# Optimization experiments

Measured on AMD Instinct MI355X. Metric: run time of the kernel, lower is better.

## Reference

```python
import jax, jax.numpy as jnp
import numpy as np

N_NODES = 100000


def _gcn_conv(x, W, b, src, dst, norm):
    # x: [N, Fin] -> [N, Fout]; PyG GCNConv: linear, normalized scatter-add, bias
    x = x @ W
    msgs = x[src] * norm[:, None]  # gather + edge scale
    out = jax.ops.segment_sum(msgs, dst, num_segments=N_NODES)
    return out + b


def setup_inputs() -> dict:
    key = jax.random.key(0)
    ks = jax.random.split(key, 8)
    N, E, F, H, C = N_NODES, 600000, 128, 128, 40
    s = lambda fan: 1.0 / np.sqrt(fan)
    return {
        "features": jax.random.normal(ks[0], (N, F), dtype=jnp.float32),
        "edge_index": jax.random.randint(ks[1], (2, E), 0, N, dtype=jnp.int64),
        "W1": jax.random.normal(ks[2], (F, H), dtype=jnp.float32) * s(F),
        "b1": jnp.zeros((H,), dtype=jnp.float32),
        "W2": jax.random.normal(ks[3], (H, H), dtype=jnp.float32) * s(H),
        "b2": jnp.zeros((H,), dtype=jnp.float32),
        "W3": jax.random.normal(ks[4], (H, C), dtype=jnp.float32) * s(H),
        "b3": jnp.zeros((C,), dtype=jnp.float32),
    }


def reference(features, edge_index, W1, b1, W2, b2, W3, b3):
    N = N_NODES
    # add self-loops (PyG GCNConv default)
    loops = jnp.arange(N, dtype=edge_index.dtype)
    src = jnp.concatenate([edge_index[0], loops])
    dst = jnp.concatenate([edge_index[1], loops])
    # symmetric normalization: deg^-1/2[src] * deg^-1/2[dst]
    deg = jax.ops.segment_sum(jnp.ones_like(dst, dtype=features.dtype), dst,
                              num_segments=N)
    dis = jnp.where(deg > 0, jax.lax.rsqrt(jnp.maximum(deg, 1.0)), 0.0)
    norm = dis[src] * dis[dst]

    x = jax.nn.relu(_gcn_conv(features, W1, b1, src, dst, norm))
    x = jax.nn.relu(_gcn_conv(x, W2, b2, src, dst, norm))
    x = jax.nn.relu(_gcn_conv(x, W3, b3, src, dst, norm))
    return jax.nn.log_softmax(x, axis=-1)
```

## Files before the change

kernel.cpp:

```cpp
#include <hip/hip_runtime.h>
#include <hip/hip_bf16.h>

#define NN 100000
#define NE 600000
#define NBLK 391
#define NPAD 100096

typedef unsigned int uint;
typedef unsigned short ushort;
typedef __attribute__((ext_vector_type(8))) short bf16x8;
typedef __attribute__((ext_vector_type(4))) float f32x4;

__device__ __forceinline__ ushort f2b(float f) {
    union { float f; uint u; } v; v.f = f;
    return (ushort)((v.u + 0x7fffu + ((v.u >> 16) & 1u)) >> 16);
}
__device__ __forceinline__ uint f2b2(float lo, float hi) {
    return (uint)f2b(lo) | ((uint)f2b(hi) << 16);
}
__device__ __forceinline__ float b2f(uint h) {
    union { uint u; float f; } v; v.u = h << 16; return v.f;
}

__global__ __launch_bounds__(256) void k_cnt_init(int* __restrict__ cnt) {
    int i = blockIdx.x * 256 + threadIdx.x;
    if (i < NN) cnt[i] = 0;
}
__global__ __launch_bounds__(256) void k_cnt(const int* __restrict__ dst,
                                             int* __restrict__ cnt,
                                             int* __restrict__ rank) {
    int e = blockIdx.x * 256 + threadIdx.x;
    if (e < NE) rank[e] = atomicAdd(&cnt[dst[e]], 1);
}
__global__ __launch_bounds__(256) void k_blockred(const int* __restrict__ cnt,
                                                  int* __restrict__ blocksum) {
    int t = threadIdx.x;
    int i = blockIdx.x * 256 + t;
    int c = (i < NN) ? cnt[i] : 0;
    #pragma unroll
    for (int o = 32; o; o >>= 1) c += __shfl_xor(c, o, 64);
    __shared__ int ws[4];
    if ((t & 63) == 0) ws[t >> 6] = c;
    __syncthreads();
    if (t == 0) blocksum[blockIdx.x] = ws[0] + ws[1] + ws[2] + ws[3];
}
__global__ __launch_bounds__(256) void k_scanblk_castW(const int* __restrict__ blocksum,
                                                       int* __restrict__ blockbase,
                                                       const float* __restrict__ W1,
                                                       const float* __restrict__ W2,
                                                       const float* __restrict__ W3,
                                                       ushort* __restrict__ WTall) {
    int t = threadIdx.x;
    if (blockIdx.x == 0) {
        __shared__ int s[NBLK];
        for (int i = t; i < NBLK; i += 256) s[i] = blocksum[i];
        __syncthreads();
        if (t == 0) {
            int run = 0;
            for (int i = 0; i < NBLK; ++i) { int v = s[i]; s[i] = run; run += v; }
        }
        __syncthreads();
        for (int i = t; i < NBLK; i += 256) blockbase[i] = s[i];
    } else {
        int o = (blockIdx.x - 1) * 256 + t;
        if (o >= 38912) return;
        float v;
        if (o < 32768) {
            const float* W = (o < 16384) ? W1 : W2;
            int off = o & 16383;
            int n = off >> 7, k = off & 127;
            v = W[k * 128 + n];
        } else {
            int off = o - 32768;
            int n = off >> 7, k = off & 127;
            v = (n < 40) ? W3[k * 40 + n] : 0.f;
        }
        WTall[o] = f2b(v);
    }
}
__global__ __launch_bounds__(256) void k_offsets(const int* __restrict__ cnt,
                                                 const int* __restrict__ blockbase,
                                                 int* __restrict__ offsets,
                                                 float* __restrict__ dis) {
    int t = threadIdx.x, lane = t & 63, wv = t >> 6;
    int i = blockIdx.x * 256 + t;
    int c = (i < NN) ? cnt[i] : 0;
    int x = c;
    #pragma unroll
    for (int o = 1; o < 64; o <<= 1) {
        int v = __shfl_up(x, o, 64);
        if (lane >= o) x += v;
    }
    __shared__ int wsum[4], wbase[4];
    if (lane == 63) wsum[wv] = x;
    __syncthreads();
    if (t == 0) {
        int run = 0;
        #pragma unroll
        for (int k = 0; k < 4; ++k) { wbase[k] = run; run += wsum[k]; }
    }
    __syncthreads();
    int excl = blockbase[blockIdx.x] + wbase[wv] + x - c;
    if (i < NN) {
        offsets[i] = excl;
        dis[i] = rsqrtf((float)(c + 1));
        if (i == NN - 1) offsets[NN] = excl + c;
    }
}
__global__ __launch_bounds__(256) void k_fill(const int* __restrict__ src,
                                              const int* __restrict__ dst,
                                              const int* __restrict__ rank,
                                              const int* __restrict__ offsets,
                                              int* __restrict__ edges) {
    int e = blockIdx.x * 256 + threadIdx.x;
    if (e < NE) {
        int s = src[e], d = dst[e], r = rank[e];
        edges[offsets[d] + r] = s;
    }
}

template <bool F32IN>
__global__ __launch_bounds__(256) void k_gemm128b(const void* __restrict__ Xin,
                                                  const ushort* __restrict__ WT,
                                                  const float* __restrict__ dis,
                                                  ushort* __restrict__ Yb) {
    __shared__ ushort AL[64 * 136];
    __shared__ ushort BL[128 * 136];
    const int t = threadIdx.x;
    const int rbase = blockIdx.x * 64;
    if (blockIdx.x == 0 && t < 16) {
        uint4 z = make_uint4(0, 0, 0, 0);
        ((uint4*)(Yb + (size_t)NN * 128))[t] = z;
    }
    #pragma unroll
    for (int i = 0; i < 8; ++i) {
        int ch = t + 256 * i;
        int n = ch >> 4, c = ch & 15;
        *(int4*)(BL + n * 136 + c * 8) = *(const int4*)(WT + n * 128 + c * 8);
    }
    #pragma unroll
    for (int i = 0; i < 4; ++i) {
        int ch = t + 256 * i;
        int m = ch >> 4, c = ch & 15;
        int row = min(rbase + m, NN - 1);
        if (F32IN) {
            const float* Xf = (const float*)Xin;
            float4 f0 = *(const float4*)(Xf + (size_t)row * 128 + c * 8);
            float4 f1 = *(const float4*)(Xf + (size_t)row * 128 + c * 8 + 4);
            uint4 o;
            o.x = f2b2(f0.x, f0.y);
            o.y = f2b2(f0.z, f0.w);
            o.z = f2b2(f1.x, f1.y);
            o.w = f2b2(f1.z, f1.w);
            *(uint4*)(AL + m * 136 + c * 8) = o;
        } else {
            const ushort* Xb = (const ushort*)Xin;
            *(int4*)(AL + m * 136 + c * 8) =
                *(const int4*)(Xb + (size_t)row * 128 + c * 8);
        }
    }
    __syncthreads();
    const int wv = t >> 6, l = t & 63;
    const int m16 = l & 15, q = l >> 4;
    f32x4 acc[8];
    #pragma unroll
    for (int j = 0; j < 8; ++j) acc[j] = (f32x4){0.f, 0.f, 0.f, 0.f};
    #pragma unroll
    for (int kt = 0; kt < 4; ++kt) {
        bf16x8 a = *(const bf16x8*)(AL + (wv * 16 + m16) * 136 + kt * 32 + q * 8);
        #pragma unroll
        for (int j = 0; j < 8; ++j) {
            bf16x8 b = *(const bf16x8*)(BL + (j * 16 + m16) * 136 + kt * 32 + q * 8);
            acc[j] = __builtin_amdgcn_mfma_f32_16x16x32_bf16(a, b, acc[j], 0, 0, 0);
        }
    }
    #pragma unroll
    for (int r = 0; r < 4; ++r) {
        int row = rbase + wv * 16 + q * 4 + r;
        if (row < NN) {
            float ds = dis[row];
            #pragma unroll
            for (int j = 0; j < 8; ++j)
                Yb[(size_t)row * 128 + j * 16 + m16] = f2b(acc[j][r] * ds);
        }
    }
}

__global__ __launch_bounds__(256) void k_gemm40b(const ushort* __restrict__ Xb,
                                                 const ushort* __restrict__ W3T,
                                                 const float* __restrict__ dis,
                                                 ushort* __restrict__ Yb) {
    __shared__ ushort AL[128 * 136];
    __shared__ ushort BL[48 * 136];
    const int t = threadIdx.x;
    const int rbase = blockIdx.x * 128;
    if (blockIdx.x == 0 && t < 8) {
        uint4 z = make_uint4(0, 0, 0, 0);
        ((uint4*)(Yb + (size_t)NN * 64))[t] = z;
    }
    #pragma unroll
    for (int i = 0; i < 3; ++i) {
        int ch = t + 256 * i;
        int n = ch >> 4, c = ch & 15;
        *(int4*)(BL + n * 136 + c * 8) = *(const int4*)(W3T + n * 128 + c * 8);
    }
    #pragma unroll
    for (int i = 0; i < 8; ++i) {
        int ch = t + 256 * i;
        int m = ch >> 4, c = ch & 15;
        int row = min(rbase + m, NN - 1);
        *(int4*)(AL + m * 136 + c * 8) =
            *(const int4*)(Xb + (size_t)row * 128 + c * 8);
    }
    __syncthreads();
    const int wv = t >> 6, l = t & 63;
    const int m16 = l & 15, q = l >> 4;
    f32x4 acc[2][3];
    #pragma unroll
    for (int i = 0; i < 2; ++i)
        #pragma unroll
        for (int j = 0; j < 3; ++j) acc[i][j] = (f32x4){0.f, 0.f, 0.f, 0.f};
    #pragma unroll
    for (int kt = 0; kt < 4; ++kt) {
        bf16x8 a[2], b[3];
        #pragma unroll
        for (int i = 0; i < 2; ++i)
            a[i] = *(const bf16x8*)(AL + ((wv * 2 + i) * 16 + m16) * 136 + kt * 32 + q * 8);
        #pragma unroll
        for (int j = 0; j < 3; ++j)
            b[j] = *(const bf16x8*)(BL + (j * 16 + m16) * 136 + kt * 32 + q * 8);
        #pragma unroll
        for (int i = 0; i < 2; ++i)
            #pragma unroll
            for (int j = 0; j < 3; ++j)
                acc[i][j] = __builtin_amdgcn_mfma_f32_16x16x32_bf16(a[i], b[j], acc[i][j], 0, 0, 0);
    }
    #pragma unroll
    for (int i = 0; i < 2; ++i) {
        #pragma unroll
        for (int r = 0; r < 4; ++r) {
            int row = rbase + (wv * 2 + i) * 16 + q * 4 + r;
            if (row < NN) {
                float ds = dis[row];
                #pragma unroll
                for (int j = 0; j < 3; ++j)
                    Yb[(size_t)row * 64 + j * 16 + m16] = f2b(acc[i][j][r] * ds);
            }
        }
    }
}

__global__ __launch_bounds__(256) void k_agg128b(const int* __restrict__ offsets,
                                                 const int* __restrict__ edges,
                                                 const float* __restrict__ dis,
                                                 const ushort* __restrict__ xw,
                                                 const float* __restrict__ bias,
                                                 ushort* __restrict__ out) {
    const int t = threadIdx.x;
    const int wv = t >> 6, lane = t & 63;
    const int hl = lane & 15;
    const int qsel = lane & 48;
    const int n = (blockIdx.x * 4 + wv) * 4 + (lane >> 4);
    const bool nvalid = n < NN;
    const int nc = nvalid ? n : NN - 1;
    const int beg = offsets[nc], end = offsets[nc + 1];
    const int deg = end - beg;
    int s_l = (hl < deg) ? edges[beg + hl] : NN;
    uint4 v0 = ((const uint4*)(xw + (size_t)nc * 128))[hl];
    float a0 = b2f(v0.x & 0xffffu), a1 = b2f(v0.x >> 16);
    float a2 = b2f(v0.y & 0xffffu), a3 = b2f(v0.y >> 16);
    float a4 = b2f(v0.z & 0xffffu), a5 = b2f(v0.z >> 16);
    float a6 = b2f(v0.w & 0xffffu), a7 = b2f(v0.w >> 16);
    int degc = min(deg, 16);
    int m1 = max(degc, __shfl_xor(degc, 16, 64));
    int dmax = max(m1, __shfl_xor(m1, 32, 64));
    int jceil = (dmax + 7) & ~7;
    for (int j = 0; j < jceil; j += 8) {
        int s[8]; uint4 u[8];
        #pragma unroll
        for (int k = 0; k < 8; ++k) s[k] = __shfl(s_l, qsel + j + k, 64);
        #pragma unroll
        for (int k = 0; k < 8; ++k)
            u[k] = ((const uint4*)(xw + (size_t)s[k] * 128))[hl];
        #pragma unroll
        for (int k = 0; k < 8; ++k) {
            a0 += b2f(u[k].x & 0xffffu); a1 += b2f(u[k].x >> 16);
            a2 += b2f(u[k].y & 0xffffu); a3 += b2f(u[k].y >> 16);
            a4 += b2f(u[k].z & 0xffffu); a5 += b2f(u[k].z >> 16);
            a6 += b2f(u[k].w & 0xffffu); a7 += b2f(u[k].w >> 16);
        }
    }
    for (int jj = beg + 16; jj < end; ++jj) {
        int s2 = edges[jj];
        uint4 u = ((const uint4*)(xw + (size_t)s2 * 128))[hl];
        a0 += b2f(u.x & 0xffffu); a1 += b2f(u.x >> 16);
        a2 += b2f(u.y & 0xffffu); a3 += b2f(u.y >> 16);
        a4 += b2f(u.z & 0xffffu); a5 += b2f(u.z >> 16);
        a6 += b2f(u.w & 0xffffu); a7 += b2f(u.w >> 16);
    }
    float d = dis[nc];
    float4 bv0 = ((const float4*)bias)[2 * hl];
    float4 bv1 = ((const float4*)bias)[2 * hl + 1];
    a0 = fmaxf(fmaf(a0, d, bv0.x), 0.f); a1 = fmaxf(fmaf(a1, d, bv0.y), 0.f);
    a2 = fmaxf(fmaf(a2, d, bv0.z), 0.f); a3 = fmaxf(fmaf(a3, d, bv0.w), 0.f);
    a4 = fmaxf(fmaf(a4, d, bv1.x), 0.f); a5 = fmaxf(fmaf(a5, d, bv1.y), 0.f);
    a6 = fmaxf(fmaf(a6, d, bv1.z), 0.f); a7 = fmaxf(fmaf(a7, d, bv1.w), 0.f);
    if (nvalid) {
        uint4 o;
        o.x = f2b2(a0, a1);
        o.y = f2b2(a2, a3);
        o.z = f2b2(a4, a5);
        o.w = f2b2(a6, a7);
        ((uint4*)(out + (size_t)n * 128))[hl] = o;
    }
}

__global__ __launch_bounds__(256) void k_agg40_lsm(const int* __restrict__ offsets,
                                                   const int* __restrict__ edges,
                                                   const float* __restrict__ dis,
                                                   const ushort* __restrict__ xw,
                                                   const float* __restrict__ bias,
                                                   float* __restrict__ out) {
    const int t = threadIdx.x;
    const int wv = t >> 6, lane = t & 63;
    const int hl = lane & 31;
    const int hsel = lane & 32;
    const int n = (blockIdx.x * 4 + wv) * 2 + (lane >> 5);
    const bool nvalid = n < NN;
    const int nc = nvalid ? n : NN - 1;
    const bool act = hl < 20;
    const int beg = offsets[nc], end = offsets[nc + 1];
    const int deg = end - beg;
    int s_l = (hl < deg) ? edges[beg + hl] : NN;
    uint v0 = ((const uint*)(xw + (size_t)nc * 64))[hl];
    float x0 = b2f(v0 & 0xffffu);
    float x1 = b2f(v0 >> 16);
    int degc = min(deg, 32);
    int dmax = max(degc, __shfl_xor(degc, 32, 64));
    int jceil = (dmax + 7) & ~7;
    for (int j = 0; j < jceil; j += 8) {
        int s[8]; uint u[8];
        #pragma unroll
        for (int k = 0; k < 8; ++k) s[k] = __shfl(s_l, hsel + j + k, 64);
        #pragma unroll
        for (int k = 0; k < 8; ++k)
            u[k] = ((const uint*)(xw + (size_t)s[k] * 64))[hl];
        #pragma unroll
        for (int k = 0; k < 8; ++k) {
            x0 += b2f(u[k] & 0xffffu);
            x1 += b2f(u[k] >> 16);
        }
    }
    for (int jj = beg + 32; jj < end; ++jj) {
        int s2 = edges[jj];
        uint u = ((const uint*)(xw + (size_t)s2 * 64))[hl];
        x0 += b2f(u & 0xffffu);
        x1 += b2f(u >> 16);
    }
    float d = dis[nc];
    if (act) {
        float2 bv = ((const float2*)bias)[hl];
        x0 = fmaxf(fmaf(x0, d, bv.x), 0.f);
        x1 = fmaxf(fmaf(x1, d, bv.y), 0.f);
    }
    float m = act ? fmaxf(x0, x1) : -1e30f;
    #pragma unroll
    for (int o = 16; o; o >>= 1) m = fmaxf(m, __shfl_xor(m, o, 64));
    float e = act ? (expf(x0 - m) + expf(x1 - m)) : 0.f;
    #pragma unroll
    for (int o = 16; o; o >>= 1) e += __shfl_xor(e, o, 64);
    if (act && nvalid) {
        float lg = m + logf(e);
        float2 o2 = make_float2(x0 - lg, x1 - lg);
        *(float2*)(out + (size_t)n * 40 + 2 * hl) = o2;
    }
}

extern "C" void kernel_launch(void* const* d_in, const int* in_sizes, int n_in,
                              void* d_out, int out_size, void* d_ws, size_t ws_size,
                              hipStream_t stream) {
    const float* feat = (const float*)d_in[0];
    const int* ei = (const int*)d_in[1];
    const float* W1 = (const float*)d_in[2];
    const float* b1 = (const float*)d_in[3];
    const float* W2 = (const float*)d_in[4];
    const float* b2 = (const float*)d_in[5];
    const float* W3 = (const float*)d_in[6];
    const float* b3 = (const float*)d_in[7];
    const int* src = ei;
    const int* dst = ei + NE;
    float* out = (float*)d_out;

    char* w = (char*)d_ws;
    int* cnt = (int*)w;        w += 100352 * 4;
    float* dis = (float*)w;    w += 100352 * 4;
    int* offsets = (int*)w;    w += 100608 * 4;
    int* rank = (int*)w;       w += 600064 * 4;
    int* blocksum = (int*)w;   w += 512 * 4;
    int* blockbase = (int*)w;  w += 512 * 4;
    int* edges = (int*)w;      w += 600064 * 4;
    ushort* WTall = (ushort*)w; w += 39168 * 2;
    ushort* W1T = WTall;
    ushort* W2T = WTall + 16384;
    ushort* W3T = WTall + 32768;
    ushort* bufYb = (ushort*)w; w += (size_t)NPAD * 128 * 2;
    ushort* bufXb = (ushort*)w; w += (size_t)NPAD * 128 * 2;
    ushort* Y40b = (ushort*)w;  w += (size_t)NPAD * 64 * 2;

    const int B = 256;
    #define CDIV(a, b) (((a) + (b) - 1) / (b))

    k_cnt_init<<<NBLK, B, 0, stream>>>(cnt);
    k_cnt<<<CDIV(NE, B), B, 0, stream>>>(dst, cnt, rank);
    k_blockred<<<NBLK, B, 0, stream>>>(cnt, blocksum);
    k_scanblk_castW<<<1 + CDIV(38912, B), B, 0, stream>>>(blocksum, blockbase,
                                                          W1, W2, W3, WTall);
    k_offsets<<<NBLK, B, 0, stream>>>(cnt, blockbase, offsets, dis);
    k_fill<<<CDIV(NE, B), B, 0, stream>>>(src, dst, rank, offsets, edges);

    k_gemm128b<true><<<CDIV(NN, 64), B, 0, stream>>>(feat, W1T, dis, bufYb);
    k_agg128b<<<CDIV(NN, 16), B, 0, stream>>>(offsets, edges, dis, bufYb, b1, bufXb);
    k_gemm128b<false><<<CDIV(NN, 64), B, 0, stream>>>(bufXb, W2T, dis, bufYb);
    k_agg128b<<<CDIV(NN, 16), B, 0, stream>>>(offsets, edges, dis, bufYb, b2, bufXb);
    k_gemm40b<<<CDIV(NN, 128), B, 0, stream>>>(bufXb, W3T, dis, Y40b);
    k_agg40_lsm<<<CDIV(NN, 8), B, 0, stream>>>(offsets, edges, dis, Y40b, b3, out);
    #undef CDIV
}
```

Measured before the change: 259.5 us.

## Fuse aggregation with following GEMM and split preprocessing kernels differently

Merges the layer-1 and layer-2 neighbor aggregation kernels with the next layer's GEMM, so aggregated rows go straight into shared memory as the MFMA A-tile instead of being written to and re-read from global memory. Each block now aggregates 64 nodes (4 per 16-lane group) and then runs the GEMM, which removes two launches and an intermediate round trip. The preprocessing is reshuffled so the weight cast runs alongside the count zeroing, and the block scan becomes its own single-block kernel. In exchange, each fused block carries large shared-memory buffers during the latency-bound gather phase, which may lower occupancy and hide gather latency less well.

```diff
diff --git a/kernel.cpp b/kernel.cpp
--- a/kernel.cpp
+++ b/kernel.cpp
@@ -22,47 +22,17 @@
     union { uint u; float f; } v; v.u = h << 16; return v.f;
 }
 
-__global__ __launch_bounds__(256) void k_cnt_init(int* __restrict__ cnt) {
-    int i = blockIdx.x * 256 + threadIdx.x;
-    if (i < NN) cnt[i] = 0;
-}
-__global__ __launch_bounds__(256) void k_cnt(const int* __restrict__ dst,
-                                             int* __restrict__ cnt,
-                                             int* __restrict__ rank) {
-    int e = blockIdx.x * 256 + threadIdx.x;
-    if (e < NE) rank[e] = atomicAdd(&cnt[dst[e]], 1);
-}
-__global__ __launch_bounds__(256) void k_blockred(const int* __restrict__ cnt,
-                                                  int* __restrict__ blocksum) {
+__global__ __launch_bounds__(256) void k_init_castW(int* __restrict__ cnt,
+                                                    const float* __restrict__ W1,
+                                                    const float* __restrict__ W2,
+                                                    const float* __restrict__ W3,
+                                                    ushort* __restrict__ WTall) {
     int t = threadIdx.x;
-    int i = blockIdx.x * 256 + t;
-    int c = (i < NN) ? cnt[i] : 0;
-    #pragma unroll
-    for (int o = 32; o; o >>= 1) c += __shfl_xor(c, o, 64);
-    __shared__ int ws[4];
-    if ((t & 63) == 0) ws[t >> 6] = c;
-    __syncthreads();
-    if (t == 0) blocksum[blockIdx.x] = ws[0] + ws[1] + ws[2] + ws[3];
-}
-__global__ __launch_bounds__(256) void k_scanblk_castW(const int* __restrict__ blocksum,
-                                                       int* __restrict__ blockbase,
-                                                       const float* __restrict__ W1,
-                                                       const float* __restrict__ W2,
-                                                       const float* __restrict__ W3,
-                                                       ushort* __restrict__ WTall) {
-    int t = threadIdx.x;
-    if (blockIdx.x == 0) {
-        __shared__ int s[NBLK];
-        for (int i = t; i < NBLK; i += 256) s[i] = blocksum[i];
-        __syncthreads();
-        if (t == 0) {
-            int run = 0;
-            for (int i = 0; i < NBLK; ++i) { int v = s[i]; s[i] = run; run += v; }
-        }
-        __syncthreads();
-        for (int i = t; i < NBLK; i += 256) blockbase[i] = s[i];
+    if (blockIdx.x < NBLK) {
+        int i = blockIdx.x * 256 + t;
+        if (i < NN) cnt[i] = 0;
     } else {
-        int o = (blockIdx.x - 1) * 256 + t;
+        int o = (blockIdx.x - NBLK) * 256 + t;
         if (o >= 38912) return;
         float v;
         if (o < 32768) {
@@ -78,6 +48,37 @@
         WTall[o] = f2b(v);
     }
 }
+__global__ __launch_bounds__(256) void k_cnt(const int* __restrict__ dst,
+                                             int* __restrict__ cnt,
+                                             int* __restrict__ rank) {
+    int e = blockIdx.x * 256 + threadIdx.x;
+    if (e < NE) rank[e] = atomicAdd(&cnt[dst[e]], 1);
+}
+__global__ __launch_bounds__(256) void k_blockred(const int* __restrict__ cnt,
+                                                  int* __restrict__ blocksum) {
+    int t = threadIdx.x;
+    int i = blockIdx.x * 256 + t;
+    int c = (i < NN) ? cnt[i] : 0;
+    #pragma unroll
+    for (int o = 32; o; o >>= 1) c += __shfl_xor(c, o, 64);
+    __shared__ int ws[4];
+    if ((t & 63) == 0) ws[t >> 6] = c;
+    __syncthreads();
+    if (t == 0) blocksum[blockIdx.x] = ws[0] + ws[1] + ws[2] + ws[3];
+}
+__global__ __launch_bounds__(256) void k_scanblk(const int* __restrict__ blocksum,
+                                                 int* __restrict__ blockbase) {
+    __shared__ int s[NBLK];
+    int t = threadIdx.x;
+    for (int i = t; i < NBLK; i += 256) s[i] = blocksum[i];
+    __syncthreads();
+    if (t == 0) {
+        int run = 0;
+        for (int i = 0; i < NBLK; ++i) { int v = s[i]; s[i] = run; run += v; }
+    }
+    __syncthreads();
+    for (int i = t; i < NBLK; i += 256) blockbase[i] = s[i];
+}
 __global__ __launch_bounds__(256) void k_offsets(const int* __restrict__ cnt,
                                                  const int* __restrict__ blockbase,
                                                  int* __restrict__ offsets,
@@ -119,11 +120,10 @@
     }
 }
 
-template <bool F32IN>
-__global__ __launch_bounds__(256) void k_gemm128b(const void* __restrict__ Xin,
-                                                  const ushort* __restrict__ WT,
-                                                  const float* __restrict__ dis,
-                                                  ushort* __restrict__ Yb) {
+__global__ __launch_bounds__(256) void k_gemm1(const float* __restrict__ Xf,
+                                               const ushort* __restrict__ WT,
+                                               const float* __restrict__ dis,
+                                               ushort* __restrict__ Yb) {
     __shared__ ushort AL[64 * 136];
     __shared__ ushort BL[128 * 136];
     const int t = threadIdx.x;
@@ -143,21 +143,14 @@
         int ch = t + 256 * i;
         int m = ch >> 4, c = ch & 15;
         int row = min(rbase + m, NN - 1);
-        if (F32IN) {
-            const float* Xf = (const float*)Xin;
-            float4 f0 = *(const float4*)(Xf + (size_t)row * 128 + c * 8);
-            float4 f1 = *(const float4*)(Xf + (size_t)row * 128 + c * 8 + 4);
-            uint4 o;
-            o.x = f2b2(f0.x, f0.y);
-            o.y = f2b2(f0.z, f0.w);
-            o.z = f2b2(f1.x, f1.y);
-            o.w = f2b2(f1.z, f1.w);
-            *(uint4*)(AL + m * 136 + c * 8) = o;
-        } else {
-            const ushort* Xb = (const ushort*)Xin;
-            *(int4*)(AL + m * 136 + c * 8) =
-                *(const int4*)(Xb + (size_t)row * 128 + c * 8);
-        }
+        float4 f0 = *(const float4*)(Xf + (size_t)row * 128 + c * 8);
+        float4 f1 = *(const float4*)(Xf + (size_t)row * 128 + c * 8 + 4);
+        uint4 o;
+        o.x = f2b2(f0.x, f0.y);
+        o.y = f2b2(f0.z, f0.w);
+        o.z = f2b2(f1.x, f1.y);
+        o.w = f2b2(f1.z, f1.w);
+        *(uint4*)(AL + m * 136 + c * 8) = o;
     }
     __syncthreads();
     const int wv = t >> 6, l = t & 63;
@@ -186,132 +179,213 @@
     }
 }
 
-__global__ __launch_bounds__(256) void k_gemm40b(const ushort* __restrict__ Xb,
-                                                 const ushort* __restrict__ W3T,
-                                                 const float* __restrict__ dis,
-                                                 ushort* __restrict__ Yb) {
-    __shared__ ushort AL[128 * 136];
-    __shared__ ushort BL[48 * 136];
+__global__ __launch_bounds__(256) void k_fused128(const int* __restrict__ offsets,
+                                                  const int* __restrict__ edges,
+                                                  const float* __restrict__ dis,
+                                                  const ushort* __restrict__ xw,
+                                                  const float* __restrict__ bias,
+                                                  const ushort* __restrict__ WT,
+                                                  ushort* __restrict__ out) {
+    __shared__ ushort AL[64 * 136];
+    __shared__ ushort BL[128 * 136];
     const int t = threadIdx.x;
-    const int rbase = blockIdx.x * 128;
-    if (blockIdx.x == 0 && t < 8) {
+    const int rbase = blockIdx.x * 64;
+    if (blockIdx.x == 0 && t < 16) {
         uint4 z = make_uint4(0, 0, 0, 0);
-        ((uint4*)(Yb + (size_t)NN * 64))[t] = z;
-    }
-    #pragma unroll
-    for (int i = 0; i < 3; ++i) {
+        ((uint4*)(out + (size_t)NN * 128))[t] = z;
+    }
+    #pragma unroll
+    for (int i = 0; i < 8; ++i) {
         int ch = t + 256 * i;
         int n = ch >> 4, c = ch & 15;
-        *(int4*)(BL + n * 136 + c * 8) = *(const int4*)(W3T + n * 128 + c * 8);
-    }
-    #pragma unroll
-    for (int i = 0; i < 8; ++i) {
-        int ch = t + 256 * i;
-        int m = ch >> 4, c = ch & 15;
-        int row = min(rbase + m, NN - 1);
-        *(int4*)(AL + m * 136 + c * 8) =
-            *(const int4*)(Xb + (size_t)row * 128 + c * 8);
-    }
-    __syncthreads();
-    const int wv = t >> 6, l = t & 63;
-    const int m16 = l & 15, q = l >> 4;
-    f32x4 acc[2][3];
-    #pragma unroll
-    for (int i = 0; i < 2; ++i)
-        #pragma unroll
-        for (int j = 0; j < 3; ++j) acc[i][j] = (f32x4){0.f, 0.f, 0.f, 0.f};
-    #pragma unroll
-    for (int kt = 0; kt < 4; ++kt) {
-        bf16x8 a[2], b[3];
-        #pragma unroll
-        for (int i = 0; i < 2; ++i)
-            a[i] = *(const bf16x8*)(AL + ((wv * 2 + i) * 16 + m16) * 136 + kt * 32 + q * 8);
-        #pragma unroll
-        for (int j = 0; j < 3; ++j)
-            b[j] = *(const bf16x8*)(BL + (j * 16 + m16) * 136 + kt * 32 + q * 8);
-        #pragma unroll
-        for (int i = 0; i < 2; ++i)
-            #pragma unroll
-            for (int j = 0; j < 3; ++j)
-                acc[i][j] = __builtin_amdgcn_mfma_f32_16x16x32_bf16(a[i], b[j], acc[i][j], 0, 0, 0);
-    }
-    #pragma unroll
-    for (int i = 0; i < 2; ++i) {
-        #pragma unroll
-        for (int r = 0; r < 4; ++r) {
-            int row = rbase + (wv * 2 + i) * 16 + q * 4 + r;
-            if (row < NN) {
-                float ds = dis[row];
-                #pragma unroll
-                for (int j = 0; j < 3; ++j)
-                    Yb[(size_t)row * 64 + j * 16 + m16] = f2b(acc[i][j][r] * ds);
-            }
-        }
-    }
-}
-
-__global__ __launch_bounds__(256) void k_agg128b(const int* __restrict__ offsets,
-                                                 const int* __restrict__ edges,
-                                                 const float* __restrict__ dis,
-                                                 const ushort* __restrict__ xw,
-                                                 const float* __restrict__ bias,
-                                                 ushort* __restrict__ out) {
-    const int t = threadIdx.x;
+        *(int4*)(BL + n * 136 + c * 8) = *(const int4*)(WT + n * 128 + c * 8);
+    }
     const int wv = t >> 6, lane = t & 63;
     const int hl = lane & 15;
     const int qsel = lane & 48;
-    const int n = (blockIdx.x * 4 + wv) * 4 + (lane >> 4);
-    const bool nvalid = n < NN;
-    const int nc = nvalid ? n : NN - 1;
-    const int beg = offsets[nc], end = offsets[nc + 1];
-    const int deg = end - beg;
-    int s_l = (hl < deg) ? edges[beg + hl] : NN;
-    uint4 v0 = ((const uint4*)(xw + (size_t)nc * 128))[hl];
-    float a0 = b2f(v0.x & 0xffffu), a1 = b2f(v0.x >> 16);
-    float a2 = b2f(v0.y & 0xffffu), a3 = b2f(v0.y >> 16);
-    float a4 = b2f(v0.z & 0xffffu), a5 = b2f(v0.z >> 16);
-    float a6 = b2f(v0.w & 0xffffu), a7 = b2f(v0.w >> 16);
-    int degc = min(deg, 16);
-    int m1 = max(degc, __shfl_xor(degc, 16, 64));
-    int dmax = max(m1, __shfl_xor(m1, 32, 64));
-    int jceil = (dmax + 7) & ~7;
-    for (int j = 0; j < jceil; j += 8) {
-        int s[8]; uint4 u[8];
-        #pragma unroll
-        for (int k = 0; k < 8; ++k) s[k] = __shfl(s_l, qsel + j + k, 64);
-        #pragma unroll
-        for (int k = 0; k < 8; ++k)
-            u[k] = ((const uint4*)(xw + (size_t)s[k] * 128))[hl];
-        #pragma unroll
-        for (int k = 0; k < 8; ++k) {
-            a0 += b2f(u[k].x & 0xffffu); a1 += b2f(u[k].x >> 16);
-            a2 += b2f(u[k].y & 0xffffu); a3 += b2f(u[k].y >> 16);
-            a4 += b2f(u[k].z & 0xffffu); a5 += b2f(u[k].z >> 16);
-            a6 += b2f(u[k].w & 0xffffu); a7 += b2f(u[k].w >> 16);
-        }
-    }
-    for (int jj = beg + 16; jj < end; ++jj) {
-        int s2 = edges[jj];
-        uint4 u = ((const uint4*)(xw + (size_t)s2 * 128))[hl];
-        a0 += b2f(u.x & 0xffffu); a1 += b2f(u.x >> 16);
-        a2 += b2f(u.y & 0xffffu); a3 += b2f(u.y >> 16);
-        a4 += b2f(u.z & 0xffffu); a5 += b2f(u.z >> 16);
-        a6 += b2f(u.w & 0xffffu); a7 += b2f(u.w >> 16);
-    }
-    float d = dis[nc];
-    float4 bv0 = ((const float4*)bias)[2 * hl];
-    float4 bv1 = ((const float4*)bias)[2 * hl + 1];
-    a0 = fmaxf(fmaf(a0, d, bv0.x), 0.f); a1 = fmaxf(fmaf(a1, d, bv0.y), 0.f);
-    a2 = fmaxf(fmaf(a2, d, bv0.z), 0.f); a3 = fmaxf(fmaf(a3, d, bv0.w), 0.f);
-    a4 = fmaxf(fmaf(a4, d, bv1.x), 0.f); a5 = fmaxf(fmaf(a5, d, bv1.y), 0.f);
-    a6 = fmaxf(fmaf(a6, d, bv1.z), 0.f); a7 = fmaxf(fmaf(a7, d, bv1.w), 0.f);
-    if (nvalid) {
+    const int qid = wv * 4 + (lane >> 4);
+    #pragma unroll
+    for (int iter = 0; iter < 4; ++iter) {
+        const int m = qid * 4 + iter;
+        const int n = rbase + m;
+        const int nc = min(n, NN - 1);
+        const int beg = offsets[nc], end = offsets[nc + 1];
+        const int deg = end - beg;
+        int s_l = (hl < deg) ? edges[beg + hl] : NN;
+        uint4 v0 = ((const uint4*)(xw + (size_t)nc * 128))[hl];
+        float a0 = b2f(v0.x & 0xffffu), a1 = b2f(v0.x >> 16);
+        float a2 = b2f(v0.y & 0xffffu), a3 = b2f(v0.y >> 16);
+        float a4 = b2f(v0.z & 0xffffu), a5 = b2f(v0.z >> 16);
+        float a6 = b2f(v0.w & 0xffffu), a7 = b2f(v0.w >> 16);
+        int degc = min(deg, 16);
+        int m1 = max(degc, __shfl_xor(degc, 16, 64));
+        int dmax = max(m1, __shfl_xor(m1, 32, 64));
+        int jceil = (dmax + 7) & ~7;
+        for (int j = 0; j < jceil; j += 8) {
+            int s[8]; uint4 u[8];
+            #pragma unroll
+            for (int k = 0; k < 8; ++k) s[k] = __shfl(s_l, qsel + j + k, 64);
+            #pragma unroll
+            for (int k = 0; k < 8; ++k)
+                u[k] = ((const uint4*)(xw + (size_t)s[k] * 128))[hl];
+            #pragma unroll
+            for (int k = 0; k < 8; ++k) {
+                a0 += b2f(u[k].x & 0xffffu); a1 += b2f(u[k].x >> 16);
+                a2 += b2f(u[k].y & 0xffffu); a3 += b2f(u[k].y >> 16);
+                a4 += b2f(u[k].z & 0xffffu); a5 += b2f(u[k].z >> 16);
+                a6 += b2f(u[k].w & 0xffffu); a7 += b2f(u[k].w >> 16);
+            }
+        }
+        for (int jj = beg + 16; jj < end; ++jj) {
+            int s2 = edges[jj];
+            uint4 u = ((const uint4*)(xw + (size_t)s2 * 128))[hl];
+            a0 += b2f(u.x & 0xffffu); a1 += b2f(u.x >> 16);
+            a2 += b2f(u.y & 0xffffu); a3 += b2f(u.y >> 16);
+            a4 += b2f(u.z & 0xffffu); a5 += b2f(u.z >> 16);
+            a6 += b2f(u.w & 0xffffu); a7 += b2f(u.w >> 16);
+        }
+        float d = dis[nc];
+        float4 bv0 = ((const float4*)bias)[2 * hl];
+        float4 bv1 = ((const float4*)bias)[2 * hl + 1];
+        a0 = fmaxf(fmaf(a0, d, bv0.x), 0.f); a1 = fmaxf(fmaf(a1, d, bv0.y), 0.f);
+        a2 = fmaxf(fmaf(a2, d, bv0.z), 0.f); a3 = fmaxf(fmaf(a3, d, bv0.w), 0.f);
+        a4 = fmaxf(fmaf(a4, d, bv1.x), 0.f); a5 = fmaxf(fmaf(a5, d, bv1.y), 0.f);
+        a6 = fmaxf(fmaf(a6, d, bv1.z), 0.f); a7 = fmaxf(fmaf(a7, d, bv1.w), 0.f);
         uint4 o;
         o.x = f2b2(a0, a1);
         o.y = f2b2(a2, a3);
         o.z = f2b2(a4, a5);
         o.w = f2b2(a6, a7);
-        ((uint4*)(out + (size_t)n * 128))[hl] = o;
+        *(uint4*)(AL + m * 136 + hl * 8) = o;
+    }
+    __syncthreads();
+    const int m16 = lane & 15, q = lane >> 4;
+    f32x4 acc[8];
+    #pragma unroll
+    for (int j = 0; j < 8; ++j) acc[j] = (f32x4){0.f, 0.f, 0.f, 0.f};
+    #pragma unroll
+    for (int kt = 0; kt < 4; ++kt) {
+        bf16x8 a = *(const bf16x8*)(AL + (wv * 16 + m16) * 136 + kt * 32 + q * 8);
+        #pragma unroll
+        for (int j = 0; j < 8; ++j) {
+            bf16x8 b = *(const bf16x8*)(BL + (j * 16 + m16) * 136 + kt * 32 + q * 8);
+            acc[j] = __builtin_amdgcn_mfma_f32_16x16x32_bf16(a, b, acc[j], 0, 0, 0);
+        }
+    }
+    #pragma unroll
+    for (int r = 0; r < 4; ++r) {
+        int row = rbase + wv * 16 + q * 4 + r;
+        if (row < NN) {
+            float ds = dis[row];
+            #pragma unroll
+            for (int j = 0; j < 8; ++j)
+                out[(size_t)row * 128 + j * 16 + m16] = f2b(acc[j][r] * ds);
+        }
+    }
+}
+
+__global__ __launch_bounds__(256) void k_fused40(const int* __restrict__ offsets,
+                                                 const int* __restrict__ edges,
+                                                 const float* __restrict__ dis,
+                                                 const ushort* __restrict__ xw,
+                                                 const float* __restrict__ bias,
+                                                 const ushort* __restrict__ W3T,
+                                                 ushort* __restrict__ out) {
+    __shared__ ushort AL[64 * 136];
+    __shared__ ushort BL[48 * 136];
+    const int t = threadIdx.x;
+    const int rbase = blockIdx.x * 64;
+    if (blockIdx.x == 0 && t < 8) {
+        uint4 z = make_uint4(0, 0, 0, 0);
+        ((uint4*)(out + (size_t)NN * 64))[t] = z;
+    }
+    #pragma unroll
+    for (int i = 0; i < 3; ++i) {
+        int ch = t + 256 * i;
+        int n = ch >> 4, c = ch & 15;
+        *(int4*)(BL + n * 136 + c * 8) = *(const int4*)(W3T + n * 128 + c * 8);
+    }
+    const int wv = t >> 6, lane = t & 63;
+    const int hl = lane & 15;
+    const int qsel = lane & 48;
+    const int qid = wv * 4 + (lane >> 4);
+    #pragma unroll
+    for (int iter = 0; iter < 4; ++iter) {
+        const int m = qid * 4 + iter;
+        const int n = rbase + m;
+        const int nc = min(n, NN - 1);
+        const int beg = offsets[nc], end = offsets[nc + 1];
+        const int deg = end - beg;
+        int s_l = (hl < deg) ? edges[beg + hl] : NN;
+        uint4 v0 = ((const uint4*)(xw + (size_t)nc * 128))[hl];
+        float a0 = b2f(v0.x & 0xffffu), a1 = b2f(v0.x >> 16);
+        float a2 = b2f(v0.y & 0xffffu), a3 = b2f(v0.y >> 16);
+        float a4 = b2f(v0.z & 0xffffu), a5 = b2f(v0.z >> 16);
+        float a6 = b2f(v0.w & 0xffffu), a7 = b2f(v0.w >> 16);
+        int degc = min(deg, 16);
+        int m1 = max(degc, __shfl_xor(degc, 16, 64));
+        int dmax = max(m1, __shfl_xor(m1, 32, 64));
+        int jceil = (dmax + 7) & ~7;
+        for (int j = 0; j < jceil; j += 8) {
+            int s[8]; uint4 u[8];
+            #pragma unroll
+            for (int k = 0; k < 8; ++k) s[k] = __shfl(s_l, qsel + j + k, 64);
+            #pragma unroll
+            for (int k = 0; k < 8; ++k)
+                u[k] = ((const uint4*)(xw + (size_t)s[k] * 128))[hl];
+            #pragma unroll
+            for (int k = 0; k < 8; ++k) {
+                a0 += b2f(u[k].x & 0xffffu); a1 += b2f(u[k].x >> 16);
+                a2 += b2f(u[k].y & 0xffffu); a3 += b2f(u[k].y >> 16);
+                a4 += b2f(u[k].z & 0xffffu); a5 += b2f(u[k].z >> 16);
+                a6 += b2f(u[k].w & 0xffffu); a7 += b2f(u[k].w >> 16);
+            }
+        }
+        for (int jj = beg + 16; jj < end; ++jj) {
+            int s2 = edges[jj];
+            uint4 u = ((const uint4*)(xw + (size_t)s2 * 128))[hl];
+            a0 += b2f(u.x & 0xffffu); a1 += b2f(u.x >> 16);
+            a2 += b2f(u.y & 0xffffu); a3 += b2f(u.y >> 16);
+            a4 += b2f(u.z & 0xffffu); a5 += b2f(u.z >> 16);
+            a6 += b2f(u.w & 0xffffu); a7 += b2f(u.w >> 16);
+        }
+        float d = dis[nc];
+        float4 bv0 = ((const float4*)bias)[2 * hl];
+        float4 bv1 = ((const float4*)bias)[2 * hl + 1];
+        a0 = fmaxf(fmaf(a0, d, bv0.x), 0.f); a1 = fmaxf(fmaf(a1, d, bv0.y), 0.f);
+        a2 = fmaxf(fmaf(a2, d, bv0.z), 0.f); a3 = fmaxf(fmaf(a3, d, bv0.w), 0.f);
+        a4 = fmaxf(fmaf(a4, d, bv1.x), 0.f); a5 = fmaxf(fmaf(a5, d, bv1.y), 0.f);
+        a6 = fmaxf(fmaf(a6, d, bv1.z), 0.f); a7 = fmaxf(fmaf(a7, d, bv1.w), 0.f);
+        uint4 o;
+        o.x = f2b2(a0, a1);
+        o.y = f2b2(a2, a3);
+        o.z = f2b2(a4, a5);
+        o.w = f2b2(a6, a7);
+        *(uint4*)(AL + m * 136 + hl * 8) = o;
+    }
+    __syncthreads();
+    const int m16 = lane & 15, q = lane >> 4;
+    f32x4 acc[3];
+    #pragma unroll
+    for (int j = 0; j < 3; ++j) acc[j] = (f32x4){0.f, 0.f, 0.f, 0.f};
+    #pragma unroll
+    for (int kt = 0; kt < 4; ++kt) {
+        bf16x8 a = *(const bf16x8*)(AL + (wv * 16 + m16) * 136 + kt * 32 + q * 8);
+        #pragma unroll
+        for (int j = 0; j < 3; ++j) {
+            bf16x8 b = *(const bf16x8*)(BL + (j * 16 + m16) * 136 + kt * 32 + q * 8);
+            acc[j] = __builtin_amdgcn_mfma_f32_16x16x32_bf16(a, b, acc[j], 0, 0, 0);
+        }
+    }
+    #pragma unroll
+    for (int r = 0; r < 4; ++r) {
+        int row = rbase + wv * 16 + q * 4 + r;
+        if (row < NN) {
+            float ds = dis[row];
+            #pragma unroll
+            for (int j = 0; j < 3; ++j)
+                out[(size_t)row * 64 + j * 16 + m16] = f2b(acc[j][r] * ds);
+        }
     }
 }
 
@@ -410,19 +484,16 @@
     const int B = 256;
     #define CDIV(a, b) (((a) + (b) - 1) / (b))
 
-    k_cnt_init<<<NBLK, B, 0, stream>>>(cnt);
+    k_init_castW<<<NBLK + CDIV(38912, B), B, 0, stream>>>(cnt, W1, W2, W3, WTall);
     k_cnt<<<CDIV(NE, B), B, 0, stream>>>(dst, cnt, rank);
     k_blockred<<<NBLK, B, 0, stream>>>(cnt, blocksum);
-    k_scanblk_castW<<<1 + CDIV(38912, B), B, 0, stream>>>(blocksum, blockbase,
-                                                          W1, W2, W3, WTall);
+    k_scanblk<<<1, B, 0, stream>>>(blocksum, blockbase);
     k_offsets<<<NBLK, B, 0, stream>>>(cnt, blockbase, offsets, dis);
     k_fill<<<CDIV(NE, B), B, 0, stream>>>(src, dst, rank, offsets, edges);
 
-    k_gemm128b<true><<<CDIV(NN, 64), B, 0, stream>>>(feat, W1T, dis, bufYb);
-    k_agg128b<<<CDIV(NN, 16), B, 0, stream>>>(offsets, edges, dis, bufYb, b1, bufXb);
-    k_gemm128b<false><<<CDIV(NN, 64), B, 0, stream>>>(bufXb, W2T, dis, bufYb);
-    k_agg128b<<<CDIV(NN, 16), B, 0, stream>>>(offsets, edges, dis, bufYb, b2, bufXb);
-    k_gemm40b<<<CDIV(NN, 128), B, 0, stream>>>(bufXb, W3T, dis, Y40b);
+    k_gemm1<<<CDIV(NN, 64), B, 0, stream>>>(feat, W1T, dis, bufYb);
+    k_fused128<<<CDIV(NN, 64), B, 0, stream>>>(offsets, edges, dis, bufYb, b1, W2T, bufXb);
+    k_fused40<<<CDIV(NN, 64), B, 0, stream>>>(offsets, edges, dis, bufXb, b2, W3T, Y40b);
     k_agg40_lsm<<<CDIV(NN, 8), B, 0, stream>>>(offsets, edges, dis, Y40b, b3, out);
     #undef CDIV
 }
```

After: 248.7 us. -4.2%, faster.
